# Kernel optimization log

Measured on AMD Instinct MI355X. Metric: run time of the kernel, lower is better.

Reference implementation:

```python
import jax, jax.numpy as jnp
import numpy as np

HEADS = 8

def _pos_enc(n, channels, dtype):
    # PositionalEncoding1D: interleaved sin/cos over node index
    inv_freq = 1.0 / (10000.0 ** (jnp.arange(0, channels, 2, dtype=jnp.float32) / channels))
    sinp = jnp.arange(n, dtype=jnp.float32)[:, None] * inv_freq[None, :]  # [n, channels//2]
    emb = jnp.stack((jnp.sin(sinp), jnp.cos(sinp)), axis=-1).reshape(n, channels)
    return emb.astype(dtype)

def _transformer_conv(x, src, dst, Wq, bq, Wk, bk, Wv, bv, Ws, bs):
    # PyG TransformerConv (concat=True, root_weight=True, eval -> no dropout)
    n = x.shape[0]
    hc = Wq.shape[1]
    c = hc // HEADS
    q = (x @ Wq + bq).reshape(n, HEADS, c)
    k = (x @ Wk + bk).reshape(n, HEADS, c)
    v = (x @ Wv + bv).reshape(n, HEADS, c)
    # per-edge attention logits, softmax grouped by target node
    logits = jnp.einsum('ehc,ehc->eh', q[dst], k[src]) / jnp.sqrt(jnp.asarray(c, x.dtype))
    m = jax.ops.segment_max(logits, dst, num_segments=n)
    e = jnp.exp(logits - m[dst])
    denom = jax.ops.segment_sum(e, dst, num_segments=n)
    alpha = e / denom[dst]  # [E, H]
    out = jax.ops.segment_sum(alpha[:, :, None] * v[src], dst, num_segments=n)
    return out.reshape(n, hc) + x @ Ws + bs

def _gcn_conv(x, src, dst, W, b):
    # PyG GCNConv: add self-loops, symmetric normalization, linear (no bias) then bias
    n = x.shape[0]
    loop = jnp.arange(n, dtype=src.dtype)
    s = jnp.concatenate([src, loop])
    d = jnp.concatenate([dst, loop])
    deg = jax.ops.segment_sum(jnp.ones(s.shape[0], x.dtype), d, num_segments=n)
    dis = jax.lax.rsqrt(jnp.maximum(deg, jnp.asarray(1.0, x.dtype)))
    norm = dis[s] * dis[d]  # [E+N]
    xw = x @ W
    return jax.ops.segment_sum(norm[:, None] * xw[s], d, num_segments=n) + b

def _forward(x, edge_index, W_embed, b_embed,
             Wq1, bq1, Wk1, bk1, Wv1, bv1, Ws1, bs1, Wh1, bh1,
             Wq2, bq2, Wk2, bk2, Wv2, bv2, Ws2, bs2, Wh2, bh2,
             Wg3, bg3, Wg4, bg4):
    src, dst = edge_index[0], edge_index[1]
    h = x @ W_embed + b_embed                       # [N, H1]
    h = h + _pos_enc(h.shape[0], h.shape[1], h.dtype)
    h = _transformer_conv(h, src, dst, Wq1, bq1, Wk1, bk1, Wv1, bv1, Ws1, bs1)
    h = h @ Wh1 + bh1
    h = _transformer_conv(h, src, dst, Wq2, bq2, Wk2, bk2, Wv2, bv2, Ws2, bs2)
    h = h @ Wh2 + bh2
    h = _gcn_conv(h, src, dst, Wg3, bg3)            # dropout is eval no-op
    h = _gcn_conv(h, src, dst, Wg4, bg4)
    return h[None]                                  # [1, N, OUT]

def setup_inputs() -> dict:
    N, E, IN, H1, H2, H3, OUT = 50000, 400000, 63, 32, 32, 32, 32
    HC = HEADS * H2
    key = jax.random.key(0)
    ks = jax.random.split(key, 32)
    p = lambda k, shp: (jax.random.normal(k, shp, dtype=jnp.float32) * 0.02)
    inp = {
        'x': jax.random.normal(ks[0], (N, IN), dtype=jnp.float32),
        'edge_index': jax.random.randint(ks[1], (2, E), 0, N, dtype=jnp.int64 if jax.config.jax_enable_x64 else jnp.int32),
        'W_embed': p(ks[2], (IN, H1)), 'b_embed': p(ks[3], (H1,)),
        'Wq1': p(ks[4], (H1, HC)), 'bq1': p(ks[5], (HC,)),
        'Wk1': p(ks[6], (H1, HC)), 'bk1': p(ks[7], (HC,)),
        'Wv1': p(ks[8], (H1, HC)), 'bv1': p(ks[9], (HC,)),
        'Ws1': p(ks[10], (H1, HC)), 'bs1': p(ks[11], (HC,)),
        'Wh1': p(ks[12], (HC, H1)), 'bh1': p(ks[13], (H1,)),
        'Wq2': p(ks[14], (H1, HC)), 'bq2': p(ks[15], (HC,)),
        'Wk2': p(ks[16], (H1, HC)), 'bk2': p(ks[17], (HC,)),
        'Wv2': p(ks[18], (H1, HC)), 'bv2': p(ks[19], (HC,)),
        'Ws2': p(ks[20], (H1, HC)), 'bs2': p(ks[21], (HC,)),
        'Wh2': p(ks[22], (HC, H1)), 'bh2': p(ks[23], (H1,)),
        'Wg3': p(ks[24], (H2, H3)), 'bg3': p(ks[25], (H3,)),
        'Wg4': p(ks[26], (H3, OUT)), 'bg4': p(ks[27], (OUT,)),
    }
    return inp

def reference(x, edge_index, W_embed, b_embed,
              Wq1, bq1, Wk1, bk1, Wv1, bv1, Ws1, bs1, Wh1, bh1,
              Wq2, bq2, Wk2, bk2, Wv2, bv2, Ws2, bs2, Wh2, bh2,
              Wg3, bg3, Wg4, bg4):
    return _forward(x, edge_index, W_embed, b_embed,
                    Wq1, bq1, Wk1, bk1, Wv1, bv1, Ws1, bs1, Wh1, bh1,
                    Wq2, bq2, Wk2, bk2, Wv2, bv2, Ws2, bs2, Wh2, bh2,
                    Wg3, bg3, Wg4, bg4)
```

## Files before the change

### kernel.cpp

```cpp
#include <hip/hip_runtime.h>
#include <cstddef>


#define NH 8
#define HCH 256
#define D32 32
#define INCH 63
#define CSCALE 0.25503485356f

__device__ __forceinline__ unsigned short f2bf(float f) {
    unsigned u = __float_as_uint(f);
    u += 0x7fff + ((u >> 16) & 1);
    return (unsigned short)(u >> 16);
}
__device__ __forceinline__ float bfu(unsigned short u) {
    return __uint_as_float(((unsigned)u) << 16);
}

__device__ const float c_invf[16] = {
    1.0f, 0.5623413251903491f, 0.31622776601683794f, 0.17782794100389228f,
    0.1f, 0.05623413251903491f, 0.031622776601683791f, 0.017782794100389228f,
    0.01f, 0.005623413251903491f, 0.0031622776601683794f, 0.0017782794100389228f,
    0.001f, 0.0005623413251903491f, 0.00031622776601683794f, 0.00017782794100389227f
};

__global__ __launch_bounds__(256) void k_embed(
    const float* __restrict__ x, const float* __restrict__ W,
    const float* __restrict__ b, float* __restrict__ H, int N, int nbMain,
    int E, const int* __restrict__ dst, int* __restrict__ cnt,
    const float* __restrict__ Wsk1, const float* __restrict__ bsk1,
    const float* __restrict__ Wh1,  const float* __restrict__ bh1,
    const float* __restrict__ Wsk2, const float* __restrict__ bsk2,
    const float* __restrict__ Wh2,  const float* __restrict__ bh2,
    float* __restrict__ WCB)
{
    if (blockIdx.x >= nbMain + 2) {
        int e = (blockIdx.x - nbMain - 2) * 256 + threadIdx.x;
        if (e < E) atomicAdd(&cnt[dst[e]], 1);
        return;
    }
    if (blockIdx.x >= nbMain) {
        int lay = blockIdx.x - nbMain;
        const float* Wsk = lay ? Wsk2 : Wsk1;
        const float* bsk = lay ? bsk2 : bsk1;
        const float* Wh  = lay ? Wh2  : Wh1;
        const float* bh  = lay ? bh2  : bh1;
        float* o = WCB + lay * 1056;
        for (int i = threadIdx.x; i < D32 * D32 + D32; i += 256) {
            if (i < D32 * D32) {
                int r = i >> 5, c = i & 31;
                float a = 0.f;
                for (int k = 0; k < HCH; ++k) a = fmaf(Wsk[r * HCH + k], Wh[k * D32 + c], a);
                o[i] = a;
            } else {
                int c = i - D32 * D32;
                float a = bh[c];
                for (int k = 0; k < HCH; ++k) a = fmaf(bsk[k], Wh[k * D32 + c], a);
                o[1024 + c] = a;
            }
        }
        return;
    }
    __shared__ float xs[8][64];
    __shared__ float ws[INCH * D32];
    int row0 = blockIdx.x * 8;
    for (int i = threadIdx.x; i < INCH * D32; i += 256) ws[i] = W[i];
    for (int i = threadIdx.x; i < 8 * INCH; i += 256) {
        int r = i / INCH, cc = i % INCH;
        int gr = row0 + r;
        xs[r][cc] = (gr < N) ? x[(size_t)gr * INCH + cc] : 0.f;
    }
    __syncthreads();
    int lr = threadIdx.x >> 5, c = threadIdx.x & 31;
    int row = row0 + lr;
    if (row >= N) return;
    float acc = b[c];
#pragma unroll
    for (int k = 0; k < INCH; ++k) acc = fmaf(xs[lr][k], ws[k * D32 + c], acc);
    float phase = (float)row * c_invf[c >> 1];
    float pe = (c & 1) ? cosf(phase) : sinf(phase);
    H[(size_t)row * D32 + c] = acc + pe;
}

__global__ void k_scan1(const int* __restrict__ cnt, int* __restrict__ rowptr,
                        int* __restrict__ partials, float* __restrict__ DIS, int N)
{
    __shared__ int s[256];
    int g = blockIdx.x * 256 + threadIdx.x;
    int myc = (g < N) ? cnt[g] : 0;
    if (g < N) DIS[g] = rsqrtf((float)myc + 1.0f);
    s[threadIdx.x] = myc;
    __syncthreads();
    for (int off = 1; off < 256; off <<= 1) {
        int t = (threadIdx.x >= off) ? s[threadIdx.x - off] : 0;
        __syncthreads();
        s[threadIdx.x] += t;
        __syncthreads();
    }
    if (g < N) rowptr[g + 1] = s[threadIdx.x];
    if (threadIdx.x == 255) partials[blockIdx.x] = s[255];
}
__global__ void k_scan2(int* __restrict__ partials, int nb) {
    __shared__ int s[256];
    int t = threadIdx.x;
    s[t] = (t < nb) ? partials[t] : 0;
    __syncthreads();
    for (int off = 1; off < 256; off <<= 1) {
        int v = (t >= off) ? s[t - off] : 0;
        __syncthreads();
        s[t] += v;
        __syncthreads();
    }
    partials[t] = (t == 0) ? 0 : s[t - 1];
}
__global__ void k_scan3b(int* __restrict__ rowptr, const int* __restrict__ partials,
                         int* __restrict__ cur, int N)
{
    int g = blockIdx.x * 256 + threadIdx.x;
    int add = partials[blockIdx.x];
    int oldprev = 0;
    if (g < N && threadIdx.x > 0) oldprev = rowptr[g];
    __syncthreads();
    if (g < N) {
        rowptr[g + 1] += add;
        cur[g] = (threadIdx.x == 0) ? add : oldprev + add;
        if (g == 0) rowptr[0] = 0;
    }
}
__global__ void k_fill(const int* __restrict__ src, const int* __restrict__ dst,
                       int* __restrict__ cur, int* __restrict__ colsrc, int E)
{
    int e = blockIdx.x * 256 + threadIdx.x;
    if (e < E) {
        int p = atomicAdd(&cur[dst[e]], 1);
        colsrc[p] = src[e];
    }
}

__global__ __launch_bounds__(256) void k_h32_to_kvqs(
    const float* __restrict__ Hm,
    const float* __restrict__ Wq, const float* __restrict__ bq,
    const float* __restrict__ Wk, const float* __restrict__ bk,
    const float* __restrict__ Wv, const float* __restrict__ bv,
    const float* __restrict__ WCBl,
    unsigned short* __restrict__ Qb, unsigned short* __restrict__ KV,
    float* __restrict__ SKIP, int N)
{
    __shared__ float hs[8][33];
    int row0 = blockIdx.x * 8;
    int c = threadIdx.x;
    {
        int r = threadIdx.x >> 5, k = threadIdx.x & 31;
        int gr = row0 + r;
        hs[r][k] = (gr < N) ? Hm[(size_t)gr * D32 + k] : 0.f;
    }
    __syncthreads();
    float aQ[8], aK[8], aV[8], aS[8];
    float bQ = bq[c], bK = bk[c], bV = bv[c];
    float bS = (c < 32) ? WCBl[1024 + c] : 0.f;
#pragma unroll
    for (int r = 0; r < 8; ++r) { aQ[r] = bQ; aK[r] = bK; aV[r] = bV; aS[r] = bS; }
#pragma unroll 8
    for (int k = 0; k < 32; ++k) {
        float wq = Wq[k * HCH + c], wk = Wk[k * HCH + c], wv = Wv[k * HCH + c];
        float wc = (c < 32) ? WCBl[k * D32 + c] : 0.f;
#pragma unroll
        for (int r = 0; r < 8; ++r) {
            float h = hs[r][k];
            aQ[r] = fmaf(h, wq, aQ[r]);
            aK[r] = fmaf(h, wk, aK[r]);
            aV[r] = fmaf(h, wv, aV[r]);
            aS[r] = fmaf(h, wc, aS[r]);
        }
    }
    int hh = c >> 5, cc = c & 31, ss = cc >> 2, ii = cc & 3;
#pragma unroll
    for (int r = 0; r < 8; ++r) {
        int gr = row0 + r;
        if (gr < N) {
            Qb[(size_t)gr * HCH + c] = f2bf(aQ[r] * CSCALE);
            size_t kb = (size_t)gr * 512 + hh * 64 + ss * 8 + ii;
            KV[kb]     = f2bf(aK[r]);
            KV[kb + 4] = f2bf(aV[r]);
            if (c < 32) SKIP[(size_t)gr * D32 + c] = aS[r];
        }
    }
}

#define PROC(A, PIDX)                                                        \
    {                                                                        \
        float f0 = __uint_as_float(A.x << 16);                               \
        float f1 = __uint_as_float(A.x & 0xffff0000u);                       \
        float f2 = __uint_as_float(A.y << 16);                               \
        float f3 = __uint_as_float(A.y & 0xffff0000u);                       \
        float t = q0 * f0 + q1 * f1 + q2 * f2 + q3 * f3;                     \
        t += __shfl_xor(t, 1, 64);                                           \
        t += __shfl_xor(t, 2, 64);                                           \
        t += __shfl_xor(t, 4, 64);                                           \
        float wg = ((PIDX) <= pl) ? exp2f(t) : 0.f;                          \
        l += wg;                                                             \
        acc0 = fmaf(wg, __uint_as_float(A.z << 16), acc0);                   \
        acc1 = fmaf(wg, __uint_as_float(A.z & 0xffff0000u), acc1);           \
        acc2 = fmaf(wg, __uint_as_float(A.w << 16), acc2);                   \
        acc3 = fmaf(wg, __uint_as_float(A.w & 0xffff0000u), acc3);           \
    }
#define CLD(B, I) colsrc[min((B) + (I), pl)]

__global__ __launch_bounds__(256) void k_attn(
    const uint4* __restrict__ KV4, const uint2* __restrict__ Qb2,
    const float* __restrict__ SKIP, float* __restrict__ H,
    const int* __restrict__ rowptr, const int* __restrict__ colsrc,
    const float* __restrict__ Wh, int N)
{
    __shared__ float os[4][264];
    int w = threadIdx.x >> 6, lane = threadIdx.x & 63;
    int d = blockIdx.x * 4 + w;
    bool act = d < N;

    float q0 = 0.f, q1 = 0.f, q2 = 0.f, q3 = 0.f;
    if (act) {
        uint2 qw = Qb2[(size_t)d * 64 + lane];
        q0 = __uint_as_float(qw.x << 16);
        q1 = __uint_as_float(qw.x & 0xffff0000u);
        q2 = __uint_as_float(qw.y << 16);
        q3 = __uint_as_float(qw.y & 0xffff0000u);
    }

    float l = 0.f, acc0 = 0.f, acc1 = 0.f, acc2 = 0.f, acc3 = 0.f;
    if (act) {
        int p0 = rowptr[d], p1 = rowptr[d + 1];
        if (p1 > p0) {
            int pl = p1 - 1;
            int s0 = CLD(p0, 0), s1 = CLD(p0, 1), s2 = CLD(p0, 2), s3 = CLD(p0, 3);
            uint4 A0 = KV4[(size_t)s0 * 64 + lane];
            uint4 A1 = KV4[(size_t)s1 * 64 + lane];
            uint4 A2 = KV4[(size_t)s2 * 64 + lane];
            uint4 A3 = KV4[(size_t)s3 * 64 + lane];
#pragma unroll 2
            for (int base = p0; base < p1; base += 4) {
                int nb2 = base + 4;
                int t0 = CLD(nb2, 0), t1 = CLD(nb2, 1), t2 = CLD(nb2, 2), t3 = CLD(nb2, 3);
                uint4 B0 = KV4[(size_t)t0 * 64 + lane];
                uint4 B1 = KV4[(size_t)t1 * 64 + lane];
                uint4 B2 = KV4[(size_t)t2 * 64 + lane];
                uint4 B3 = KV4[(size_t)t3 * 64 + lane];
                PROC(A0, base)
                PROC(A1, base + 1)
                PROC(A2, base + 2)
                PROC(A3, base + 3)
                A0 = B0; A1 = B1; A2 = B2; A3 = B3;
            }
        }
        float inv = (l > 0.f) ? 1.f / l : 0.f;
        int gch = (lane >> 3) * 32 + (lane & 7) * 4;
        os[w][gch + 0] = acc0 * inv;
        os[w][gch + 1] = acc1 * inv;
        os[w][gch + 2] = acc2 * inv;
        os[w][gch + 3] = acc3 * inv;
    }
    __syncthreads();

    if (act) {
        int c = lane & 31, half = lane >> 5;
        float a2 = half ? 0.f : SKIP[(size_t)d * D32 + c];
        int kb = half * 128;
#pragma unroll 8
        for (int kk = 0; kk < 128; ++kk)
            a2 = fmaf(os[w][kb + kk], Wh[(kb + kk) * D32 + c], a2);
        a2 += __shfl_xor(a2, 32, 64);
        if (lane < 32) H[(size_t)d * D32 + c] = a2;
    }
}

__global__ __launch_bounds__(256) void k_xw3(
    const float* __restrict__ X, const float* __restrict__ W,
    const float* __restrict__ DIS, unsigned short* __restrict__ O, int N)
{
    __shared__ float xs[8][33];
    __shared__ float ws[D32 * D32];
    int row0 = blockIdx.x * 8;
    int c = threadIdx.x & 31, lr = threadIdx.x >> 5;
    for (int i = threadIdx.x; i < D32 * D32; i += 256) ws[i] = W[i];
    {
        int gr = row0 + lr;
        xs[lr][c] = (gr < N) ? X[(size_t)gr * D32 + c] : 0.f;
    }
    __syncthreads();
    int row = row0 + lr;
    if (row >= N) return;
    float acc = 0.f;
#pragma unroll
    for (int k = 0; k < D32; ++k) acc = fmaf(xs[lr][k], ws[k * D32 + c], acc);
    O[(size_t)row * D32 + c] = f2bf(DIS[row] * acc);
}

__global__ __launch_bounds__(256) void k_gcn_f(
    const unsigned short* __restrict__ XWp, const float* __restrict__ DIS,
    const int* __restrict__ rowptr, const int* __restrict__ colsrc,
    const float* __restrict__ bg, const float* __restrict__ Wg4,
    unsigned short* __restrict__ XWout, int N)
{
    __shared__ float wgs[1024];
    for (int i = threadIdx.x; i < 1024; i += 256) wgs[i] = Wg4[i];
    __syncthreads();
    int g = threadIdx.x >> 5;
    int c = threadIdx.x & 31;
    int d = blockIdx.x * 8 + g;
    bool act = d < N;
    float dd = 0.f, h3 = 0.f;
    if (act) {
        float acc = bfu(XWp[(size_t)d * D32 + c]);
        int p0 = rowptr[d], p1 = rowptr[d + 1];
        if (p1 > p0) {
            int pl = p1 - 1;
            unsigned short uA = XWp[(size_t)CLD(p0, 0) * D32 + c];
            unsigned short uB = XWp[(size_t)CLD(p0, 1) * D32 + c];
            unsigned short uC = XWp[(size_t)CLD(p0, 2) * D32 + c];
            unsigned short uD = XWp[(size_t)CLD(p0, 3) * D32 + c];
#pragma unroll 4
            for (int p = p0; p < p1; ++p) {
                unsigned short uN = XWp[(size_t)CLD(p, 4) * D32 + c];
                acc += bfu(uA);
                uA = uB; uB = uC; uC = uD; uD = uN;
            }
        }
        dd = DIS[d];
        h3 = dd * acc + bg[c];
    }
    float s = 0.f;
#pragma unroll
    for (int k = 0; k < 32; ++k)
        s = fmaf(__shfl(h3, k, 32), wgs[k * D32 + c], s);
    if (act) XWout[(size_t)d * D32 + c] = f2bf(dd * s);
}

__global__ __launch_bounds__(256) void k_gcn_last(
    const unsigned short* __restrict__ XWp, const float* __restrict__ DIS,
    const int* __restrict__ rowptr, const int* __restrict__ colsrc,
    const float* __restrict__ bg, float* __restrict__ Out, int N)
{
    int g = threadIdx.x >> 5;
    int c = threadIdx.x & 31;
    int d = blockIdx.x * 8 + g;
    if (d >= N) return;
    float acc = bfu(XWp[(size_t)d * D32 + c]);
    int p0 = rowptr[d], p1 = rowptr[d + 1];
    if (p1 > p0) {
        int pl = p1 - 1;
        unsigned short uA = XWp[(size_t)CLD(p0, 0) * D32 + c];
        unsigned short uB = XWp[(size_t)CLD(p0, 1) * D32 + c];
        unsigned short uC = XWp[(size_t)CLD(p0, 2) * D32 + c];
        unsigned short uD = XWp[(size_t)CLD(p0, 3) * D32 + c];
#pragma unroll 4
        for (int p = p0; p < p1; ++p) {
            unsigned short uN = XWp[(size_t)CLD(p, 4) * D32 + c];
            acc += bfu(uA);
            uA = uB; uB = uC; uC = uD; uD = uN;
        }
    }
    Out[(size_t)d * D32 + c] = DIS[d] * acc + bg[c];
}

extern "C" void kernel_launch(void* const* d_in, const int* in_sizes, int n_in,
                              void* d_out, int out_size, void* d_ws, size_t ws_size,
                              hipStream_t stream)
{
    const float* x  = (const float*)d_in[0];
    const int*   ei = (const int*)d_in[1];
    const int N = in_sizes[0] / INCH;
    const int E = in_sizes[1] / 2;
    const int* src = ei;
    const int* dst = ei + E;

    const float* W_embed = (const float*)d_in[2];
    const float* b_embed = (const float*)d_in[3];
    const float* Wg3 = (const float*)d_in[24];
    const float* bg3 = (const float*)d_in[25];
    const float* Wg4 = (const float*)d_in[26];
    const float* bg4 = (const float*)d_in[27];

    unsigned short* KV  = (unsigned short*)d_ws;
    unsigned short* Qb  = KV + (size_t)N * 512;
    float* H      = (float*)(Qb + (size_t)N * HCH);
    float* SKIP   = H + (size_t)N * D32;
    unsigned short* XW1 = (unsigned short*)(SKIP + (size_t)N * D32);
    unsigned short* XW2 = XW1 + (size_t)N * D32;
    int*   rowptr = (int*)(XW2 + (size_t)N * D32);
    int*   colsrc = rowptr + (N + 1);
    int*   cursor = colsrc + E;
    int*   partials = cursor + N;
    float* DIS    = (float*)(partials + 256);
    float* WCB    = DIS + N;
    float* out    = (float*)d_out;

    const int nb8 = (N + 7) / 8;
    const int nbN = (N + 255) / 256;
    const int nbE = (E + 255) / 256;

    hipMemsetAsync(cursor, 0, (size_t)N * sizeof(int), stream);

    k_embed<<<nb8 + 2 + nbE, 256, 0, stream>>>(
        x, W_embed, b_embed, H, N, nb8, E, dst, cursor,
        (const float*)d_in[10], (const float*)d_in[11],
        (const float*)d_in[12], (const float*)d_in[13],
        (const float*)d_in[20], (const float*)d_in[21],
        (const float*)d_in[22], (const float*)d_in[23], WCB);

    k_scan1<<<nbN, 256, 0, stream>>>(cursor, rowptr, partials, DIS, N);
    k_scan2<<<1, 256, 0, stream>>>(partials, nbN);
    k_scan3b<<<nbN, 256, 0, stream>>>(rowptr, partials, cursor, N);
    k_fill<<<nbE, 256, 0, stream>>>(src, dst, cursor, colsrc, E);

    for (int layer = 0; layer < 2; ++layer) {
        int base = 4 + layer * 10;
        const float* Wq = (const float*)d_in[base + 0];
        const float* bq = (const float*)d_in[base + 1];
        const float* Wk = (const float*)d_in[base + 2];
        const float* bk = (const float*)d_in[base + 3];
        const float* Wv = (const float*)d_in[base + 4];
        const float* bv = (const float*)d_in[base + 5];
        const float* Wh = (const float*)d_in[base + 8];

        k_h32_to_kvqs<<<nb8, 256, 0, stream>>>(
            H, Wq, bq, Wk, bk, Wv, bv, WCB + layer * 1056, Qb, KV, SKIP, N);
        k_attn<<<(N + 3) / 4, 256, 0, stream>>>(
            (const uint4*)KV, (const uint2*)Qb, SKIP, H, rowptr, colsrc, Wh, N);
    }

    k_xw3<<<nb8, 256, 0, stream>>>(H, Wg3, DIS, XW1, N);
    k_gcn_f<<<nb8, 256, 0, stream>>>(XW1, DIS, rowptr, colsrc, bg3, Wg4, XW2, N);
    k_gcn_last<<<nb8, 256, 0, stream>>>(XW2, DIS, rowptr, colsrc, bg4, out, N);
}
```

Measured before the change: 434.3 us.

## Use bf16 dot2 in attention, 16-row projection tiles, two-way split GCN gathers

The attention inner product now uses v_dot2_f32_bf16 inline asm on packed bf16 query/key words and the raw exp2 builtin, removing the unpack and FMA work per edge. The QKV projection kernel processes 16 rows per block instead of 8, so each weight load is reused across more rows at the cost of more registers. Both GCN aggregation kernels now give each destination node a full wavefront, with each half of the lanes gathering alternate edges and the halves combined by a shuffle. This doubles gather parallelism per node but halves the nodes per block.

Measured after the change: 466.0 us. 1.07x slower.

```diff
diff --git a/kernel.cpp b/kernel.cpp
--- a/kernel.cpp
+++ b/kernel.cpp
@@ -146,26 +146,26 @@
     unsigned short* __restrict__ Qb, unsigned short* __restrict__ KV,
     float* __restrict__ SKIP, int N)
 {
-    __shared__ float hs[8][33];
-    int row0 = blockIdx.x * 8;
+    __shared__ float hs[16][33];
+    int row0 = blockIdx.x * 16;
     int c = threadIdx.x;
-    {
-        int r = threadIdx.x >> 5, k = threadIdx.x & 31;
+    for (int i = threadIdx.x; i < 16 * 32; i += 256) {
+        int r = i >> 5, k = i & 31;
         int gr = row0 + r;
         hs[r][k] = (gr < N) ? Hm[(size_t)gr * D32 + k] : 0.f;
     }
     __syncthreads();
-    float aQ[8], aK[8], aV[8], aS[8];
+    float aQ[16], aK[16], aV[16], aS[16];
     float bQ = bq[c], bK = bk[c], bV = bv[c];
     float bS = (c < 32) ? WCBl[1024 + c] : 0.f;
 #pragma unroll
-    for (int r = 0; r < 8; ++r) { aQ[r] = bQ; aK[r] = bK; aV[r] = bV; aS[r] = bS; }
+    for (int r = 0; r < 16; ++r) { aQ[r] = bQ; aK[r] = bK; aV[r] = bV; aS[r] = bS; }
 #pragma unroll 8
     for (int k = 0; k < 32; ++k) {
         float wq = Wq[k * HCH + c], wk = Wk[k * HCH + c], wv = Wv[k * HCH + c];
         float wc = (c < 32) ? WCBl[k * D32 + c] : 0.f;
 #pragma unroll
-        for (int r = 0; r < 8; ++r) {
+        for (int r = 0; r < 16; ++r) {
             float h = hs[r][k];
             aQ[r] = fmaf(h, wq, aQ[r]);
             aK[r] = fmaf(h, wk, aK[r]);
@@ -175,7 +175,7 @@
     }
     int hh = c >> 5, cc = c & 31, ss = cc >> 2, ii = cc & 3;
 #pragma unroll
-    for (int r = 0; r < 8; ++r) {
+    for (int r = 0; r < 16; ++r) {
         int gr = row0 + r;
         if (gr < N) {
             Qb[(size_t)gr * HCH + c] = f2bf(aQ[r] * CSCALE);
@@ -189,15 +189,15 @@
 
 #define PROC(A, PIDX)                                                        \
     {                                                                        \
-        float f0 = __uint_as_float(A.x << 16);                               \
-        float f1 = __uint_as_float(A.x & 0xffff0000u);                       \
-        float f2 = __uint_as_float(A.y << 16);                               \
-        float f3 = __uint_as_float(A.y & 0xffff0000u);                       \
-        float t = q0 * f0 + q1 * f1 + q2 * f2 + q3 * f3;                     \
+        float t1, t;                                                         \
+        asm("v_dot2_f32_bf16 %0, %1, %2, %3"                                 \
+            : "=v"(t1) : "v"(A.y), "v"(qy), "v"(zf));                        \
+        asm("v_dot2_f32_bf16 %0, %1, %2, %3"                                 \
+            : "=v"(t) : "v"(A.x), "v"(qx), "v"(t1));                         \
         t += __shfl_xor(t, 1, 64);                                           \
         t += __shfl_xor(t, 2, 64);                                           \
         t += __shfl_xor(t, 4, 64);                                           \
-        float wg = ((PIDX) <= pl) ? exp2f(t) : 0.f;                          \
+        float wg = ((PIDX) <= pl) ? __builtin_amdgcn_exp2f(t) : 0.f;         \
         l += wg;                                                             \
         acc0 = fmaf(wg, __uint_as_float(A.z << 16), acc0);                   \
         acc1 = fmaf(wg, __uint_as_float(A.z & 0xffff0000u), acc1);           \
@@ -217,14 +217,12 @@
     int d = blockIdx.x * 4 + w;
     bool act = d < N;
 
-    float q0 = 0.f, q1 = 0.f, q2 = 0.f, q3 = 0.f;
+    unsigned qx = 0u, qy = 0u;
     if (act) {
         uint2 qw = Qb2[(size_t)d * 64 + lane];
-        q0 = __uint_as_float(qw.x << 16);
-        q1 = __uint_as_float(qw.x & 0xffff0000u);
-        q2 = __uint_as_float(qw.y << 16);
-        q3 = __uint_as_float(qw.y & 0xffff0000u);
-    }
+        qx = qw.x; qy = qw.y;
+    }
+    float zf = 0.f;
 
     float l = 0.f, acc0 = 0.f, acc1 = 0.f, acc2 = 0.f, acc3 = 0.f;
     if (act) {
@@ -239,11 +237,11 @@
 #pragma unroll 2
             for (int base = p0; base < p1; base += 4) {
                 int nb2 = base + 4;
-                int t0 = CLD(nb2, 0), t1 = CLD(nb2, 1), t2 = CLD(nb2, 2), t3 = CLD(nb2, 3);
+                int t0 = CLD(nb2, 0), t1c = CLD(nb2, 1), t2c = CLD(nb2, 2), t3c = CLD(nb2, 3);
                 uint4 B0 = KV4[(size_t)t0 * 64 + lane];
-                uint4 B1 = KV4[(size_t)t1 * 64 + lane];
-                uint4 B2 = KV4[(size_t)t2 * 64 + lane];
-                uint4 B3 = KV4[(size_t)t3 * 64 + lane];
+                uint4 B1 = KV4[(size_t)t1c * 64 + lane];
+                uint4 B2 = KV4[(size_t)t2c * 64 + lane];
+                uint4 B3 = KV4[(size_t)t3c * 64 + lane];
                 PROC(A0, base)
                 PROC(A1, base + 1)
                 PROC(A2, base + 2)
@@ -303,35 +301,36 @@
     __shared__ float wgs[1024];
     for (int i = threadIdx.x; i < 1024; i += 256) wgs[i] = Wg4[i];
     __syncthreads();
-    int g = threadIdx.x >> 5;
-    int c = threadIdx.x & 31;
-    int d = blockIdx.x * 8 + g;
+    int w = threadIdx.x >> 6, lane = threadIdx.x & 63;
+    int c = lane & 31, half = lane >> 5;
+    int d = blockIdx.x * 4 + w;
     bool act = d < N;
-    float dd = 0.f, h3 = 0.f;
+    float acc = 0.f;
     if (act) {
-        float acc = bfu(XWp[(size_t)d * D32 + c]);
+        if (half == 0) acc = bfu(XWp[(size_t)d * D32 + c]);
         int p0 = rowptr[d], p1 = rowptr[d + 1];
-        if (p1 > p0) {
+        int i0 = p0 + half;
+        if (i0 < p1) {
             int pl = p1 - 1;
-            unsigned short uA = XWp[(size_t)CLD(p0, 0) * D32 + c];
-            unsigned short uB = XWp[(size_t)CLD(p0, 1) * D32 + c];
-            unsigned short uC = XWp[(size_t)CLD(p0, 2) * D32 + c];
-            unsigned short uD = XWp[(size_t)CLD(p0, 3) * D32 + c];
-#pragma unroll 4
-            for (int p = p0; p < p1; ++p) {
-                unsigned short uN = XWp[(size_t)CLD(p, 4) * D32 + c];
+            unsigned short uA = XWp[(size_t)colsrc[min(i0,     pl)] * D32 + c];
+            unsigned short uB = XWp[(size_t)colsrc[min(i0 + 2, pl)] * D32 + c];
+            unsigned short uC = XWp[(size_t)colsrc[min(i0 + 4, pl)] * D32 + c];
+            unsigned short uD = XWp[(size_t)colsrc[min(i0 + 6, pl)] * D32 + c];
+            for (int p = i0; p < p1; p += 2) {
+                unsigned short uN = XWp[(size_t)colsrc[min(p + 8, pl)] * D32 + c];
                 acc += bfu(uA);
                 uA = uB; uB = uC; uC = uD; uD = uN;
             }
         }
-        dd = DIS[d];
-        h3 = dd * acc + bg[c];
-    }
+    }
+    acc += __shfl_xor(acc, 32, 64);
+    float dd = 0.f, h3 = 0.f;
+    if (act) { dd = DIS[d]; h3 = dd * acc + bg[c]; }
     float s = 0.f;
 #pragma unroll
     for (int k = 0; k < 32; ++k)
         s = fmaf(__shfl(h3, k, 32), wgs[k * D32 + c], s);
-    if (act) XWout[(size_t)d * D32 + c] = f2bf(dd * s);
+    if (act && half == 0) XWout[(size_t)d * D32 + c] = f2bf(dd * s);
 }
 
 __global__ __launch_bounds__(256) void k_gcn_last(
@@ -339,26 +338,28 @@
     const int* __restrict__ rowptr, const int* __restrict__ colsrc,
     const float* __restrict__ bg, float* __restrict__ Out, int N)
 {
-    int g = threadIdx.x >> 5;
-    int c = threadIdx.x & 31;
-    int d = blockIdx.x * 8 + g;
+    int w = threadIdx.x >> 6, lane = threadIdx.x & 63;
+    int c = lane & 31, half = lane >> 5;
+    int d = blockIdx.x * 4 + w;
     if (d >= N) return;
-    float acc = bfu(XWp[(size_t)d * D32 + c]);
+    float acc = 0.f;
+    if (half == 0) acc = bfu(XWp[(size_t)d * D32 + c]);
     int p0 = rowptr[d], p1 = rowptr[d + 1];
-    if (p1 > p0) {
+    int i0 = p0 + half;
+    if (i0 < p1) {
         int pl = p1 - 1;
-        unsigned short uA = XWp[(size_t)CLD(p0, 0) * D32 + c];
-        unsigned short uB = XWp[(size_t)CLD(p0, 1) * D32 + c];
-        unsigned short uC = XWp[(size_t)CLD(p0, 2) * D32 + c];
-        unsigned short uD = XWp[(size_t)CLD(p0, 3) * D32 + c];
-#pragma unroll 4
-        for (int p = p0; p < p1; ++p) {
-            unsigned short uN = XWp[(size_t)CLD(p, 4) * D32 + c];
+        unsigned short uA = XWp[(size_t)colsrc[min(i0,     pl)] * D32 + c];
+        unsigned short uB = XWp[(size_t)colsrc[min(i0 + 2, pl)] * D32 + c];
+        unsigned short uC = XWp[(size_t)colsrc[min(i0 + 4, pl)] * D32 + c];
+        unsigned short uD = XWp[(size_t)colsrc[min(i0 + 6, pl)] * D32 + c];
+        for (int p = i0; p < p1; p += 2) {
+            unsigned short uN = XWp[(size_t)colsrc[min(p + 8, pl)] * D32 + c];
             acc += bfu(uA);
             uA = uB; uB = uC; uC = uD; uD = uN;
         }
     }
-    Out[(size_t)d * D32 + c] = DIS[d] * acc + bg[c];
+    acc += __shfl_xor(acc, 32, 64);
+    if (half == 0) Out[(size_t)d * D32 + c] = DIS[d] * acc + bg[c];
 }
 
 extern "C" void kernel_launch(void* const* d_in, const int* in_sizes, int n_in,
@@ -393,9 +394,11 @@
     float* WCB    = DIS + N;
     float* out    = (float*)d_out;
 
-    const int nb8 = (N + 7) / 8;
-    const int nbN = (N + 255) / 256;
-    const int nbE = (E + 255) / 256;
+    const int nb8  = (N + 7) / 8;
+    const int nb16 = (N + 15) / 16;
+    const int nb4  = (N + 3) / 4;
+    const int nbN  = (N + 255) / 256;
+    const int nbE  = (E + 255) / 256;
 
     hipMemsetAsync(cursor, 0, (size_t)N * sizeof(int), stream);
 
@@ -421,13 +424,13 @@
         const float* bv = (const float*)d_in[base + 5];
         const float* Wh = (const float*)d_in[base + 8];
 
-        k_h32_to_kvqs<<<nb8, 256, 0, stream>>>(
+        k_h32_to_kvqs<<<nb16, 256, 0, stream>>>(
             H, Wq, bq, Wk, bk, Wv, bv, WCB + layer * 1056, Qb, KV, SKIP, N);
-        k_attn<<<(N + 3) / 4, 256, 0, stream>>>(
+        k_attn<<<nb4, 256, 0, stream>>>(
             (const uint4*)KV, (const uint2*)Qb, SKIP, H, rowptr, colsrc, Wh, N);
     }
 
     k_xw3<<<nb8, 256, 0, stream>>>(H, Wg3, DIS, XW1, N);
-    k_gcn_f<<<nb8, 256, 0, stream>>>(XW1, DIS, rowptr, colsrc, bg3, Wg4, XW2, N);
-    k_gcn_last<<<nb8, 256, 0, stream>>>(XW2, DIS, rowptr, colsrc, bg4, out, N);
-}
+    k_gcn_f<<<nb4, 256, 0, stream>>>(XW1, DIS, rowptr, colsrc, bg3, Wg4, XW2, N);
+    k_gcn_last<<<nb4, 256, 0, stream>>>(XW2, DIS, rowptr, colsrc, bg4, out, N);
+}
```
